# Optimization experiments

Measured on AMD Instinct MI355X. Metric: run time of the kernel, lower is better.

Reference implementation:

```python
import jax, jax.numpy as jnp
import numpy as np

VARIANCE = (0.1, 0.2)
THRESHOLD = 0.5
NEG_POS = 3


def point_form(boxes):
    # (cx,cy,w,h) -> (xmin,ymin,xmax,ymax)
    return jnp.concatenate([boxes[:, :2] - boxes[:, 2:] / 2,
                            boxes[:, :2] + boxes[:, 2:] / 2], axis=1)


def jaccard(a, b):
    # a: [T,4] xyxy truths, b: [P,4] xyxy priors -> IoU [T,P]
    lt = jnp.maximum(a[:, None, :2], b[None, :, :2])
    rb = jnp.minimum(a[:, None, 2:], b[None, :, 2:])
    wh = jnp.clip(rb - lt, 0.0)
    inter = wh[..., 0] * wh[..., 1]
    area_a = ((a[:, 2] - a[:, 0]) * (a[:, 3] - a[:, 1]))[:, None]
    area_b = ((b[:, 2] - b[:, 0]) * (b[:, 3] - b[:, 1]))[None, :]
    return inter / (area_a + area_b - inter)


def encode(matched, priors):
    g_cxcy = (matched[:, :2] + matched[:, 2:]) / 2 - priors[:, :2]
    g_cxcy = g_cxcy / (VARIANCE[0] * priors[:, 2:])
    g_wh = jnp.log((matched[:, 2:] - matched[:, :2]) / priors[:, 2:]) / VARIANCE[1]
    return jnp.concatenate([g_cxcy, g_wh], axis=1)


def match_one(truths, priors):
    # SSD match for one image; labels are zeroed in BiBoxLoss -> binary conf {0,1}
    overlaps = jaccard(truths, point_form(priors))          # [T,P]
    best_prior_idx = jnp.argmax(overlaps, axis=1)           # [T]
    best_truth_overlap = jnp.max(overlaps, axis=0)          # [P]
    best_truth_idx = jnp.argmax(overlaps, axis=0)           # [P]
    best_truth_overlap = best_truth_overlap.at[best_prior_idx].set(2.0)
    best_truth_idx = best_truth_idx.at[best_prior_idx].set(
        jnp.arange(truths.shape[0]))
    matched = truths[best_truth_idx]                        # [P,4]
    conf = jnp.where(best_truth_overlap < THRESHOLD, 0, 1)  # [P] int
    loc = encode(matched, priors)
    return loc, conf


def bibox_loss(loc_data, conf_data, priors, targets):
    num, num_priors = loc_data.shape[0], loc_data.shape[1]
    truths = targets[..., :4]                               # [B,T,4]
    loc_t, conf_t = jax.vmap(lambda t: match_one(t, priors))(truths)

    pos = conf_t > 0                                        # [B,P]
    # smooth L1 (sum) over positive priors
    ad = jnp.abs(loc_data - loc_t)
    sl1 = jnp.where(ad < 1.0, 0.5 * ad * ad, ad - 0.5)
    loss_l = jnp.sum(sl1 * pos[..., None].astype(loc_data.dtype))

    # per-prior CE (logsumexp - gathered logit) for hard-negative mining
    lse = jax.nn.logsumexp(conf_data, axis=-1)              # [B,P]
    gathered = jnp.take_along_axis(conf_data, conf_t[..., None], axis=-1)[..., 0]
    loss_c_all = lse - gathered                             # [B,P]

    loss_c_mine = jnp.where(pos, 0.0, loss_c_all)
    loss_idx = jnp.argsort(-loss_c_mine, axis=1)
    idx_rank = jnp.argsort(loss_idx, axis=1)                # rank of each prior
    num_pos = jnp.sum(pos.astype(jnp.int32), axis=1, keepdims=True)  # [B,1]
    num_neg = jnp.minimum(NEG_POS * num_pos, num_priors - 1)
    neg = idx_rank < num_neg                                # [B,P]

    sel = pos | neg
    loss_c = jnp.sum(jnp.where(sel, loss_c_all, 0.0))

    N = jnp.sum(num_pos).astype(loc_data.dtype)
    return loss_l / N, loss_c / N


def setup_inputs() -> dict:
    key = jax.random.key(0)
    k1, k2, k3, k4, k5, k6 = jax.random.split(key, 6)
    B, P, T = 32, 65536, 16
    loc_data = jax.random.normal(k1, (B, P, 4), dtype=jnp.float32)
    conf_data = jax.random.normal(k2, (B, P, 2), dtype=jnp.float32)
    # priors: valid center-form boxes
    pc = 0.15 + 0.7 * jax.random.uniform(k3, (P, 2), dtype=jnp.float32)
    pwh = 0.05 + 0.25 * jax.random.uniform(k4, (P, 2), dtype=jnp.float32)
    priors = jnp.concatenate([pc, pwh], axis=1)
    # targets: valid corner-form boxes + dummy label column (zeroed by the loss)
    tc = 0.2 + 0.6 * jax.random.uniform(k5, (B, T, 2), dtype=jnp.float32)
    twh = 0.05 + 0.25 * jax.random.uniform(k6, (B, T, 2), dtype=jnp.float32)
    boxes = jnp.concatenate([tc - twh / 2, tc + twh / 2], axis=-1)
    targets = jnp.concatenate(
        [boxes, jnp.ones((B, T, 1), dtype=jnp.float32)], axis=-1)
    return {"loc_data": loc_data, "conf_data": conf_data,
            "priors": priors, "targets": targets}


def reference(loc_data, conf_data, priors, targets):
    return bibox_loss(loc_data, conf_data, priors, targets)
```

## Files before the change

kernel.cpp:

```cpp
#include <hip/hip_runtime.h>

#define NB_ 32
#define NP_ 65536
#define NT_ 16
#define HB 1024
#define HSCALE 128.0f
#define NBX 32
#define CHUNKS 2

__device__ __forceinline__ float softplus_(float x) {
    return fmaxf(x, 0.0f) + __logf(1.0f + __expf(-fabsf(x)));
}

__device__ __forceinline__ float iou_fast(float tx0, float ty0, float tx1, float ty1, float ta,
                                          float bx0, float by0, float bx1, float by1, float ar) {
    float lx = fmaxf(tx0, bx0), ly = fmaxf(ty0, by0);
    float rx = fminf(tx1, bx1), ry = fminf(ty1, by1);
    float w = fmaxf(rx - lx, 0.0f), h = fmaxf(ry - ly, 0.0f);
    float inter = w * h;
    return __fdividef(inter, ta + ar - inter);
}

__global__ void __launch_bounds__(256) mainK(
    const float* __restrict__ loc, const float* __restrict__ conf,
    const float* __restrict__ priors, const float* __restrict__ targets,
    int* __restrict__ gcnt, float* __restrict__ gsum,
    unsigned long long* __restrict__ bestPart,
    float* __restrict__ part_ll, float* __restrict__ part_pc, int* __restrict__ part_np,
    unsigned* __restrict__ ticket)
{
    const int bx = blockIdx.x, b = blockIdx.y, tid = threadIdx.x;

    __shared__ float tr[NT_][5];
    __shared__ int hc[HB];
    __shared__ float hs[HB];
    __shared__ unsigned wkey[4][NT_], wp[4][NT_];
    __shared__ float sh_ll[4], sh_pc[4];
    __shared__ int sh_np[4];

    if (b == 0 && bx == 0 && tid == 0) *ticket = 0u;

    for (int i = tid; i < HB; i += 256) { hc[i] = 0; hs[i] = 0.0f; }
    if (tid < NT_) {
        const float* tp = targets + ((size_t)b * NT_ + tid) * 5;
        float x0 = tp[0], y0 = tp[1], x1 = tp[2], y1 = tp[3];
        tr[tid][0] = x0; tr[tid][1] = y0; tr[tid][2] = x1; tr[tid][3] = y1;
        tr[tid][4] = (x1 - x0) * (y1 - y0);
    }
    __syncthreads();

    float ll_acc = 0.0f, pc_acc = 0.0f;
    int np_acc = 0;
    unsigned tkey[NT_];
#pragma unroll
    for (int t = 0; t < NT_; t++) tkey[t] = 0u;

    for (int c = 0; c < CHUNKS; c++) {
        const int pbase = (bx * CHUNKS + c) * 1024 + tid;
        float4 pr[4];
        float pbx0[4], pby0[4], pbx1[4], pby1[4], par[4];
#pragma unroll
        for (int i = 0; i < 4; i++) {
            pr[i] = ((const float4*)priors)[pbase + 256 * i];
            float hw = pr[i].z * 0.5f, hh = pr[i].w * 0.5f;
            pbx0[i] = pr[i].x - hw; pby0[i] = pr[i].y - hh;
            pbx1[i] = pr[i].x + hw; pby1[i] = pr[i].y + hh;
            par[i] = (pbx1[i] - pbx0[i]) * (pby1[i] - pby0[i]);
        }
        unsigned pkey[4] = {0u, 0u, 0u, 0u};
#pragma unroll
        for (int t = 0; t < NT_; t++) {
            float tx0 = tr[t][0], ty0 = tr[t][1], tx1 = tr[t][2], ty1 = tr[t][3], ta = tr[t][4];
            unsigned lowt = (unsigned)(15 - t);
            unsigned lowc = (unsigned)(15 - c * 4);
#pragma unroll
            for (int i = 0; i < 4; i++) {
                float iou = iou_fast(tx0, ty0, tx1, ty1, ta,
                                     pbx0[i], pby0[i], pbx1[i], pby1[i], par[i]);
                unsigned base = (__float_as_uint(iou) & 0xFFFFFFFCu) << 2;
                unsigned kt = base | lowt;
                unsigned kp = base | (lowc - (unsigned)i);
                pkey[i] = (kt > pkey[i]) ? kt : pkey[i];
                tkey[t] = (kp > tkey[t]) ? kp : tkey[t];
            }
        }
#pragma unroll
        for (int i = 0; i < 4; i++) {
            int p = pbase + 256 * i;
            size_t bp = (size_t)b * NP_ + p;
            bool pos = (pkey[i] >= 0xFC000000u);
            float2 cxy = ((const float2*)conf)[bp];
            float dd = cxy.y - cxy.x;
            float v = pos ? 0.0f : softplus_(dd);
            int bin = min(HB - 1, (int)(v * HSCALE));
            atomicAdd(&hc[bin], 1);
            atomicAdd(&hs[bin], v);
            if (pos) {
                np_acc++;
                pc_acc += softplus_(-dd);
                int t = 15 - (int)(pkey[i] & 15u);
                float tx0 = tr[t][0], ty0 = tr[t][1], tx1 = tr[t][2], ty1 = tr[t][3];
                float gcx = ((tx0 + tx1) * 0.5f - pr[i].x) / (0.1f * pr[i].z);
                float gcy = ((ty0 + ty1) * 0.5f - pr[i].y) / (0.1f * pr[i].w);
                float gw = __logf((tx1 - tx0) / pr[i].z) * 5.0f;
                float gh = __logf((ty1 - ty0) / pr[i].w) * 5.0f;
                float4 ld = ((const float4*)loc)[bp];
                float d0 = fabsf(ld.x - gcx), d1 = fabsf(ld.y - gcy);
                float d2 = fabsf(ld.z - gw),  d3 = fabsf(ld.w - gh);
                ll_acc += (d0 < 1.0f) ? 0.5f * d0 * d0 : d0 - 0.5f;
                ll_acc += (d1 < 1.0f) ? 0.5f * d1 * d1 : d1 - 0.5f;
                ll_acc += (d2 < 1.0f) ? 0.5f * d2 * d2 : d2 - 0.5f;
                ll_acc += (d3 < 1.0f) ? 0.5f * d3 * d3 : d3 - 0.5f;
            }
        }
    }

    const int wave = tid >> 6, lane = tid & 63;
#pragma unroll
    for (int t = 0; t < NT_; t++) {
        unsigned k = tkey[t], m = k;
        for (int off = 32; off > 0; off >>= 1) {
            unsigned o = __shfl_down(m, off, 64);
            m = (o > m) ? o : m;
        }
        m = __shfl(m, 0, 64);
        unsigned long long ball = __ballot(k == m);
        if (lane == 0) {
            int l = __ffsll((long long)ball) - 1;
            int ci = 15 - (int)(m & 15u);
            int p = bx * (CHUNKS * 1024) + ci * 256 + wave * 64 + l;
            wkey[wave][t] = m;
            wp[wave][t] = (unsigned)p;
        }
    }
    for (int off = 32; off > 0; off >>= 1) {
        ll_acc += __shfl_down(ll_acc, off, 64);
        pc_acc += __shfl_down(pc_acc, off, 64);
        np_acc += __shfl_down(np_acc, off, 64);
    }
    if (lane == 0) { sh_ll[wave] = ll_acc; sh_pc[wave] = pc_acc; sh_np[wave] = np_acc; }
    __syncthreads();

    if (tid < NT_) {
        unsigned bk = wkey[0][tid], bpv = wp[0][tid];
        for (int w = 1; w < 4; w++) {
            unsigned k2 = wkey[w][tid], p2 = wp[w][tid];
            if (k2 > bk || (k2 == bk && p2 < bpv)) { bk = k2; bpv = p2; }
        }
        unsigned long long pk = (((unsigned long long)bk) << 32) | (unsigned)(~bpv);
        bestPart[((size_t)b * NT_ + tid) * NBX + bx] = pk;
    }
    if (tid == 0) {
        part_ll[b * NBX + bx] = sh_ll[0] + sh_ll[1] + sh_ll[2] + sh_ll[3];
        part_pc[b * NBX + bx] = sh_pc[0] + sh_pc[1] + sh_pc[2] + sh_pc[3];
        part_np[b * NBX + bx] = sh_np[0] + sh_np[1] + sh_np[2] + sh_np[3];
    }
    int* gc = gcnt + ((size_t)(b * NBX + bx)) * HB;
    float* gs = gsum + ((size_t)(b * NBX + bx)) * HB;
    for (int i = tid; i < HB; i += 256) { gc[i] = hc[i]; gs[i] = hs[i]; }
}

__global__ void __launch_bounds__(1024) finishK(
    const float* __restrict__ loc, const float* __restrict__ conf,
    const float* __restrict__ priors, const float* __restrict__ targets,
    const int* __restrict__ gcnt, const float* __restrict__ gsum,
    const unsigned long long* __restrict__ bestPart,
    const float* __restrict__ part_ll, const float* __restrict__ part_pc,
    const int* __restrict__ part_np,
    float* __restrict__ final_l, float* __restrict__ final_c, int* __restrict__ final_n,
    unsigned* __restrict__ ticket, float* __restrict__ out)
{
    const int b = blockIdx.x, tid = threadIdx.x;
    __shared__ int hc[HB];
    __shared__ float hs[HB];
    __shared__ float tr[NT_][5];
    __shared__ unsigned ps[NT_];
    __shared__ float s_dll, s_dpc;
    __shared__ int s_dnp;
    __shared__ unsigned ccnt[16];
    __shared__ float csm[16];
    __shared__ int s_last;

    if (tid == 0) { s_dll = 0.0f; s_dpc = 0.0f; s_dnp = 0; s_last = 0; }
    if (tid < NT_) {
        const float* tp = targets + ((size_t)b * NT_ + tid) * 5;
        float x0 = tp[0], y0 = tp[1], x1 = tp[2], y1 = tp[3];
        tr[tid][0] = x0; tr[tid][1] = y0; tr[tid][2] = x1; tr[tid][3] = y1;
        tr[tid][4] = (x1 - x0) * (y1 - y0);
    }
    {
        int i = tid;
        int c = 0; float s = 0.0f;
#pragma unroll
        for (int j = 0; j < NBX; j++) {
            c += gcnt[((size_t)(b * NBX + j)) * HB + i];
            s += gsum[((size_t)(b * NBX + j)) * HB + i];
        }
        hc[i] = c; hs[i] = s;
    }
    if (tid < NT_) {
        unsigned long long v = bestPart[((size_t)b * NT_ + tid) * NBX];
        for (int j = 1; j < NBX; j++) {
            unsigned long long u = bestPart[((size_t)b * NT_ + tid) * NBX + j];
            if (u > v) v = u;
        }
        ps[tid] = ~((unsigned)(v & 0xffffffffULL));
    }
    __syncthreads();

    if (tid < NT_) {
        unsigned p = ps[tid];
        bool active = true;
        for (int u = tid + 1; u < NT_; u++)
            if (ps[u] == p) { active = false; break; }
        if (active) {
            float4 prv = ((const float4*)priors)[p];
            float hw = prv.z * 0.5f, hh = prv.w * 0.5f;
            float qx0 = prv.x - hw, qy0 = prv.y - hh;
            float qx1 = prv.x + hw, qy1 = prv.y + hh;
            float areab = (qx1 - qx0) * (qy1 - qy0);
            unsigned pk = 0u;
            for (int tt = 0; tt < NT_; tt++) {
                float iou = iou_fast(tr[tt][0], tr[tt][1], tr[tt][2], tr[tt][3], tr[tt][4],
                                     qx0, qy0, qx1, qy1, areab);
                unsigned cand = ((__float_as_uint(iou) & 0xFFFFFFFCu) << 2)
                              | (unsigned)(15 - tt);
                pk = (cand > pk) ? cand : pk;
            }
            bool pos0 = (pk >= 0xFC000000u);
            int t0 = 15 - (int)(pk & 15u);
            size_t bp = (size_t)b * NP_ + p;
            float2 cxy = ((const float2*)conf)[bp];
            float dd = cxy.y - cxy.x;
            float4 ld = ((const float4*)loc)[bp];

            auto sl1_of = [&](int tt) -> float {
                float tx0 = tr[tt][0], ty0 = tr[tt][1], tx1 = tr[tt][2], ty1 = tr[tt][3];
                float gcx = ((tx0 + tx1) * 0.5f - prv.x) / (0.1f * prv.z);
                float gcy = ((ty0 + ty1) * 0.5f - prv.y) / (0.1f * prv.w);
                float gw = __logf((tx1 - tx0) / prv.z) * 5.0f;
                float gh = __logf((ty1 - ty0) / prv.w) * 5.0f;
                float d0 = fabsf(ld.x - gcx), d1 = fabsf(ld.y - gcy);
                float d2 = fabsf(ld.z - gw),  d3 = fabsf(ld.w - gh);
                float s = (d0 < 1.0f) ? 0.5f * d0 * d0 : d0 - 0.5f;
                s += (d1 < 1.0f) ? 0.5f * d1 * d1 : d1 - 0.5f;
                s += (d2 < 1.0f) ? 0.5f * d2 * d2 : d2 - 0.5f;
                s += (d3 < 1.0f) ? 0.5f * d3 * d3 : d3 - 0.5f;
                return s;
            };
            float dll = sl1_of(tid) - (pos0 ? sl1_of(t0) : 0.0f);
            atomicAdd(&s_dll, dll);
            if (!pos0) {
                float v = softplus_(dd);
                int bin = min(HB - 1, (int)(v * HSCALE));
                atomicSub(&hc[bin], 1);
                atomicAdd(&hs[bin], -v);
                atomicAdd(&s_dpc, softplus_(-dd));
                atomicAdd(&s_dnp, 1);
            }
        }
    }
    __syncthreads();

    if (tid < 16) {
        unsigned cacc = 0; float sacc = 0.0f;
        for (int j = 0; j < 64; j++) { cacc += (unsigned)hc[tid * 64 + j]; sacc += hs[tid * 64 + j]; }
        ccnt[tid] = cacc; csm[tid] = sacc;
    }
    __syncthreads();

    if (tid == 0) {
        float sll = s_dll, spc = s_dpc;
        int n = s_dnp;
        for (int j = 0; j < NBX; j++) {
            sll += part_ll[b * NBX + j];
            spc += part_pc[b * NBX + j];
            n += part_np[b * NBX + j];
        }
        int K = 3 * n;
        if (K > NP_ - 1) K = NP_ - 1;
        float tk = 0.0f;
        if (K > 0) {
            unsigned need = (unsigned)K, cum = 0;
            float s = 0.0f;
            int cb = 15;
            for (; cb > 0; --cb) {
                if (cum + ccnt[cb] >= need) break;
                cum += ccnt[cb]; s += csm[cb];
            }
            int bin = cb * 64 + 63;
            for (; bin > cb * 64; --bin) {
                if (cum + (unsigned)hc[bin] >= need) break;
                cum += (unsigned)hc[bin]; s += hs[bin];
            }
            unsigned rem = need - cum;
            int cv = hc[bin];
            float avg = (cv > 0) ? __fdividef(hs[bin], (float)cv) : 0.0f;
            tk = s + (float)rem * avg;
        }
        final_l[b] = sll;
        final_c[b] = spc + tk;
        final_n[b] = n;
        __threadfence();
        unsigned old = atomicAdd(ticket, 1u);
        if (old == NB_ - 1) s_last = 1;
    }
    __syncthreads();

    if (s_last) {
        __threadfence();
        if (tid < 64) {
            float lv = 0.0f, cv = 0.0f;
            int nv = 0;
            if (tid < NB_) { lv = final_l[tid]; cv = final_c[tid]; nv = final_n[tid]; }
            for (int off = 32; off > 0; off >>= 1) {
                lv += __shfl_down(lv, off, 64);
                cv += __shfl_down(cv, off, 64);
                nv += __shfl_down(nv, off, 64);
            }
            if (tid == 0) {
                float fn = (float)nv;
                out[0] = lv / fn;
                out[1] = cv / fn;
            }
        }
    }
}

extern "C" void kernel_launch(void* const* d_in, const int* in_sizes, int n_in,
                              void* d_out, int out_size, void* d_ws, size_t ws_size,
                              hipStream_t stream) {
    const float* loc = (const float*)d_in[0];
    const float* conf = (const float*)d_in[1];
    const float* priors = (const float*)d_in[2];
    const float* targets = (const float*)d_in[3];
    float* out = (float*)d_out;

    char* w = (char*)d_ws;
    int* gcnt = (int*)w;
    float* gsum = (float*)(w + (4u << 20));
    char* acc = w + (8u << 20);
    unsigned long long* bestPart = (unsigned long long*)acc;
    float* part_ll = (float*)(acc + (128u << 10));
    float* part_pc = (float*)(acc + (128u << 10) + 4096);
    int* part_np   = (int*)(acc + (128u << 10) + 8192);
    float* final_l = (float*)(acc + (128u << 10) + 12288);
    float* final_c = (float*)(acc + (128u << 10) + 12416);
    int* final_n   = (int*)(acc + (128u << 10) + 12544);
    unsigned* ticket = (unsigned*)(acc + (128u << 10) + 12672);

    mainK<<<dim3(NBX, NB_), 256, 0, stream>>>(loc, conf, priors, targets,
                                              gcnt, gsum, bestPart,
                                              part_ll, part_pc, part_np, ticket);
    finishK<<<NB_, 1024, 0, stream>>>(loc, conf, priors, targets, gcnt, gsum, bestPart,
                                      part_ll, part_pc, part_np,
                                      final_l, final_c, final_n, ticket, out);
}
```

Measured before the change: 148.8 us.

## Double mainK grid to one chunk per block and store histogram counts as u16

Removes the per-block chunk loop so each of twice as many blocks handles 1024 priors, which doubles the grid to 64x32 blocks for more parallelism and latency hiding. The partial count histograms shrink from int to unsigned short to offset the doubled per-block histogram traffic. Priors are reloaded from global memory for positive matches instead of being kept in registers. The cost is that finishK must reduce twice as many partial histograms and best-prior candidates per image, and the workspace layout is shifted to fit.

```diff
diff --git a/kernel.cpp b/kernel.cpp
--- a/kernel.cpp
+++ b/kernel.cpp
@@ -5,8 +5,7 @@
 #define NT_ 16
 #define HB 1024
 #define HSCALE 128.0f
-#define NBX 32
-#define CHUNKS 2
+#define NBX 64
 
 __device__ __forceinline__ float softplus_(float x) {
     return fmaxf(x, 0.0f) + __logf(1.0f + __expf(-fabsf(x)));
@@ -24,14 +23,15 @@
 __global__ void __launch_bounds__(256) mainK(
     const float* __restrict__ loc, const float* __restrict__ conf,
     const float* __restrict__ priors, const float* __restrict__ targets,
-    int* __restrict__ gcnt, float* __restrict__ gsum,
+    unsigned short* __restrict__ gcnt, float* __restrict__ gsum,
     unsigned long long* __restrict__ bestPart,
     float* __restrict__ part_ll, float* __restrict__ part_pc, int* __restrict__ part_np,
     unsigned* __restrict__ ticket)
 {
     const int bx = blockIdx.x, b = blockIdx.y, tid = threadIdx.x;
 
-    __shared__ float tr[NT_][5];
+    __shared__ float4 trb[NT_];
+    __shared__ float tra[NT_];
     __shared__ int hc[HB];
     __shared__ float hs[HB];
     __shared__ unsigned wkey[4][NT_], wp[4][NT_];
@@ -44,74 +44,73 @@
     if (tid < NT_) {
         const float* tp = targets + ((size_t)b * NT_ + tid) * 5;
         float x0 = tp[0], y0 = tp[1], x1 = tp[2], y1 = tp[3];
-        tr[tid][0] = x0; tr[tid][1] = y0; tr[tid][2] = x1; tr[tid][3] = y1;
-        tr[tid][4] = (x1 - x0) * (y1 - y0);
-    }
-    __syncthreads();
+        trb[tid] = make_float4(x0, y0, x1, y1);
+        tra[tid] = (x1 - x0) * (y1 - y0);
+    }
+    __syncthreads();
+
+    const int pbase = bx * 1024 + tid;
+    float pbx0[4], pby0[4], pbx1[4], pby1[4], par[4];
+#pragma unroll
+    for (int i = 0; i < 4; i++) {
+        float4 pr = ((const float4*)priors)[pbase + 256 * i];
+        float hw = pr.z * 0.5f, hh = pr.w * 0.5f;
+        pbx0[i] = pr.x - hw; pby0[i] = pr.y - hh;
+        pbx1[i] = pr.x + hw; pby1[i] = pr.y + hh;
+        par[i] = (pbx1[i] - pbx0[i]) * (pby1[i] - pby0[i]);
+    }
+
+    unsigned pkey[4] = {0u, 0u, 0u, 0u};
+    unsigned tkey[NT_];
+#pragma unroll
+    for (int t = 0; t < NT_; t++) tkey[t] = 0u;
+
+#pragma unroll
+    for (int t = 0; t < NT_; t++) {
+        float4 tb = trb[t];
+        float ta = tra[t];
+#pragma unroll
+        for (int i = 0; i < 4; i++) {
+            float iou = iou_fast(tb.x, tb.y, tb.z, tb.w, ta,
+                                 pbx0[i], pby0[i], pbx1[i], pby1[i], par[i]);
+            unsigned base = (__float_as_uint(iou) & 0xFFFFFFFCu) << 2;
+            unsigned kt = base | (unsigned)(15 - t);
+            unsigned kp = base | (unsigned)(15 - i);
+            pkey[i] = (kt > pkey[i]) ? kt : pkey[i];
+            tkey[t] = (kp > tkey[t]) ? kp : tkey[t];
+        }
+    }
 
     float ll_acc = 0.0f, pc_acc = 0.0f;
     int np_acc = 0;
-    unsigned tkey[NT_];
-#pragma unroll
-    for (int t = 0; t < NT_; t++) tkey[t] = 0u;
-
-    for (int c = 0; c < CHUNKS; c++) {
-        const int pbase = (bx * CHUNKS + c) * 1024 + tid;
-        float4 pr[4];
-        float pbx0[4], pby0[4], pbx1[4], pby1[4], par[4];
-#pragma unroll
-        for (int i = 0; i < 4; i++) {
-            pr[i] = ((const float4*)priors)[pbase + 256 * i];
-            float hw = pr[i].z * 0.5f, hh = pr[i].w * 0.5f;
-            pbx0[i] = pr[i].x - hw; pby0[i] = pr[i].y - hh;
-            pbx1[i] = pr[i].x + hw; pby1[i] = pr[i].y + hh;
-            par[i] = (pbx1[i] - pbx0[i]) * (pby1[i] - pby0[i]);
-        }
-        unsigned pkey[4] = {0u, 0u, 0u, 0u};
-#pragma unroll
-        for (int t = 0; t < NT_; t++) {
-            float tx0 = tr[t][0], ty0 = tr[t][1], tx1 = tr[t][2], ty1 = tr[t][3], ta = tr[t][4];
-            unsigned lowt = (unsigned)(15 - t);
-            unsigned lowc = (unsigned)(15 - c * 4);
-#pragma unroll
-            for (int i = 0; i < 4; i++) {
-                float iou = iou_fast(tx0, ty0, tx1, ty1, ta,
-                                     pbx0[i], pby0[i], pbx1[i], pby1[i], par[i]);
-                unsigned base = (__float_as_uint(iou) & 0xFFFFFFFCu) << 2;
-                unsigned kt = base | lowt;
-                unsigned kp = base | (lowc - (unsigned)i);
-                pkey[i] = (kt > pkey[i]) ? kt : pkey[i];
-                tkey[t] = (kp > tkey[t]) ? kp : tkey[t];
-            }
-        }
-#pragma unroll
-        for (int i = 0; i < 4; i++) {
-            int p = pbase + 256 * i;
-            size_t bp = (size_t)b * NP_ + p;
-            bool pos = (pkey[i] >= 0xFC000000u);
-            float2 cxy = ((const float2*)conf)[bp];
-            float dd = cxy.y - cxy.x;
-            float v = pos ? 0.0f : softplus_(dd);
-            int bin = min(HB - 1, (int)(v * HSCALE));
-            atomicAdd(&hc[bin], 1);
-            atomicAdd(&hs[bin], v);
-            if (pos) {
-                np_acc++;
-                pc_acc += softplus_(-dd);
-                int t = 15 - (int)(pkey[i] & 15u);
-                float tx0 = tr[t][0], ty0 = tr[t][1], tx1 = tr[t][2], ty1 = tr[t][3];
-                float gcx = ((tx0 + tx1) * 0.5f - pr[i].x) / (0.1f * pr[i].z);
-                float gcy = ((ty0 + ty1) * 0.5f - pr[i].y) / (0.1f * pr[i].w);
-                float gw = __logf((tx1 - tx0) / pr[i].z) * 5.0f;
-                float gh = __logf((ty1 - ty0) / pr[i].w) * 5.0f;
-                float4 ld = ((const float4*)loc)[bp];
-                float d0 = fabsf(ld.x - gcx), d1 = fabsf(ld.y - gcy);
-                float d2 = fabsf(ld.z - gw),  d3 = fabsf(ld.w - gh);
-                ll_acc += (d0 < 1.0f) ? 0.5f * d0 * d0 : d0 - 0.5f;
-                ll_acc += (d1 < 1.0f) ? 0.5f * d1 * d1 : d1 - 0.5f;
-                ll_acc += (d2 < 1.0f) ? 0.5f * d2 * d2 : d2 - 0.5f;
-                ll_acc += (d3 < 1.0f) ? 0.5f * d3 * d3 : d3 - 0.5f;
-            }
+#pragma unroll
+    for (int i = 0; i < 4; i++) {
+        int p = pbase + 256 * i;
+        size_t bp = (size_t)b * NP_ + p;
+        bool pos = (pkey[i] >= 0xFC000000u);
+        float2 cxy = ((const float2*)conf)[bp];
+        float dd = cxy.y - cxy.x;
+        float v = pos ? 0.0f : softplus_(dd);
+        int bin = min(HB - 1, (int)(v * HSCALE));
+        atomicAdd(&hc[bin], 1);
+        atomicAdd(&hs[bin], v);
+        if (pos) {
+            np_acc++;
+            pc_acc += softplus_(-dd);
+            int t = 15 - (int)(pkey[i] & 15u);
+            float4 tb = trb[t];
+            float4 prv = ((const float4*)priors)[p];
+            float gcx = ((tb.x + tb.z) * 0.5f - prv.x) / (0.1f * prv.z);
+            float gcy = ((tb.y + tb.w) * 0.5f - prv.y) / (0.1f * prv.w);
+            float gw = __logf((tb.z - tb.x) / prv.z) * 5.0f;
+            float gh = __logf((tb.w - tb.y) / prv.w) * 5.0f;
+            float4 ld = ((const float4*)loc)[bp];
+            float d0 = fabsf(ld.x - gcx), d1 = fabsf(ld.y - gcy);
+            float d2 = fabsf(ld.z - gw),  d3 = fabsf(ld.w - gh);
+            ll_acc += (d0 < 1.0f) ? 0.5f * d0 * d0 : d0 - 0.5f;
+            ll_acc += (d1 < 1.0f) ? 0.5f * d1 * d1 : d1 - 0.5f;
+            ll_acc += (d2 < 1.0f) ? 0.5f * d2 * d2 : d2 - 0.5f;
+            ll_acc += (d3 < 1.0f) ? 0.5f * d3 * d3 : d3 - 0.5f;
         }
     }
 
@@ -128,7 +127,7 @@
         if (lane == 0) {
             int l = __ffsll((long long)ball) - 1;
             int ci = 15 - (int)(m & 15u);
-            int p = bx * (CHUNKS * 1024) + ci * 256 + wave * 64 + l;
+            int p = bx * 1024 + ci * 256 + wave * 64 + l;
             wkey[wave][t] = m;
             wp[wave][t] = (unsigned)p;
         }
@@ -155,15 +154,15 @@
         part_pc[b * NBX + bx] = sh_pc[0] + sh_pc[1] + sh_pc[2] + sh_pc[3];
         part_np[b * NBX + bx] = sh_np[0] + sh_np[1] + sh_np[2] + sh_np[3];
     }
-    int* gc = gcnt + ((size_t)(b * NBX + bx)) * HB;
+    unsigned short* gc = gcnt + ((size_t)(b * NBX + bx)) * HB;
     float* gs = gsum + ((size_t)(b * NBX + bx)) * HB;
-    for (int i = tid; i < HB; i += 256) { gc[i] = hc[i]; gs[i] = hs[i]; }
+    for (int i = tid; i < HB; i += 256) { gc[i] = (unsigned short)hc[i]; gs[i] = hs[i]; }
 }
 
 __global__ void __launch_bounds__(1024) finishK(
     const float* __restrict__ loc, const float* __restrict__ conf,
     const float* __restrict__ priors, const float* __restrict__ targets,
-    const int* __restrict__ gcnt, const float* __restrict__ gsum,
+    const unsigned short* __restrict__ gcnt, const float* __restrict__ gsum,
     const unsigned long long* __restrict__ bestPart,
     const float* __restrict__ part_ll, const float* __restrict__ part_pc,
     const int* __restrict__ part_np,
@@ -193,7 +192,7 @@
         int c = 0; float s = 0.0f;
 #pragma unroll
         for (int j = 0; j < NBX; j++) {
-            c += gcnt[((size_t)(b * NBX + j)) * HB + i];
+            c += (int)gcnt[((size_t)(b * NBX + j)) * HB + i];
             s += gsum[((size_t)(b * NBX + j)) * HB + i];
         }
         hc[i] = c; hs[i] = s;
@@ -337,17 +336,17 @@
     float* out = (float*)d_out;
 
     char* w = (char*)d_ws;
-    int* gcnt = (int*)w;
+    unsigned short* gcnt = (unsigned short*)w;
     float* gsum = (float*)(w + (4u << 20));
-    char* acc = w + (8u << 20);
+    char* acc = w + (12u << 20);
     unsigned long long* bestPart = (unsigned long long*)acc;
-    float* part_ll = (float*)(acc + (128u << 10));
-    float* part_pc = (float*)(acc + (128u << 10) + 4096);
-    int* part_np   = (int*)(acc + (128u << 10) + 8192);
-    float* final_l = (float*)(acc + (128u << 10) + 12288);
-    float* final_c = (float*)(acc + (128u << 10) + 12416);
-    int* final_n   = (int*)(acc + (128u << 10) + 12544);
-    unsigned* ticket = (unsigned*)(acc + (128u << 10) + 12672);
+    float* part_ll = (float*)(acc + 262144);
+    float* part_pc = (float*)(acc + 262144 + 8192);
+    int* part_np   = (int*)(acc + 262144 + 16384);
+    float* final_l = (float*)(acc + 262144 + 24576);
+    float* final_c = (float*)(acc + 262144 + 24704);
+    int* final_n   = (int*)(acc + 262144 + 24832);
+    unsigned* ticket = (unsigned*)(acc + 262144 + 24960);
 
     mainK<<<dim3(NBX, NB_), 256, 0, stream>>>(loc, conf, priors, targets,
                                               gcnt, gsum, bestPart,
```

Result: no change. 151.1 us (+1.5%).
